# Kernel tuning notes

Hardware: AMD Instinct MI355X
Metric: run time of the kernel (lower is better)

The kernel has to match this reference:

```python
import jax, jax.numpy as jnp
import numpy as np

N = 50000       # nodes
E = 800000      # directed edges (src -> dst)
INDIM, HID, OUT = 256, 128, 64
NEG_SLOPE = 0.2  # PyG GATConv default negative_slope


def gat_layer(x, src, dst, W, a_src, a_dst, b, n_nodes):
    """Single-head PyG-style GATConv with self-loops already in (src, dst)."""
    h = x @ W.T                                   # [N, F_out]
    alpha_src = h @ a_src                         # [N]
    alpha_dst = h @ a_dst                         # [N]
    # per-edge attention logits, LeakyReLU
    e = jax.nn.leaky_relu(alpha_src[src] + alpha_dst[dst], NEG_SLOPE)  # [E']
    # segment softmax grouped by destination node (numerically stable)
    m = jnp.full((n_nodes,), -jnp.inf, e.dtype).at[dst].max(e)
    ee = jnp.exp(e - m[dst])
    denom = jax.ops.segment_sum(ee, dst, num_segments=n_nodes)
    alpha = ee / denom[dst]                       # [E']
    # weighted scatter-add of source messages
    out = jax.ops.segment_sum(h[src] * alpha[:, None], dst, num_segments=n_nodes)
    return out + b


def setup_inputs() -> dict:
    key = jax.random.key(0)
    ks = jax.random.split(key, 10)
    s = 0.1
    return {
        "x": jax.random.normal(ks[0], (N, INDIM), jnp.float32),
        "edge_index": jax.random.randint(ks[1], (2, E), 0, N, dtype=jnp.int32),
        "W1": jax.random.normal(ks[2], (HID, INDIM), jnp.float32) * s,
        "a_src1": jax.random.normal(ks[3], (HID,), jnp.float32) * s,
        "a_dst1": jax.random.normal(ks[4], (HID,), jnp.float32) * s,
        "b1": jnp.zeros((HID,), jnp.float32),
        "W2": jax.random.normal(ks[5], (OUT, HID), jnp.float32) * s,
        "a_src2": jax.random.normal(ks[6], (OUT,), jnp.float32) * s,
        "a_dst2": jax.random.normal(ks[7], (OUT,), jnp.float32) * s,
        "b2": jnp.zeros((OUT,), jnp.float32),
    }


def reference(x, edge_index, W1, a_src1, a_dst1, b1, W2, a_src2, a_dst2, b2):
    n_nodes = x.shape[0]
    # PyG GATConv default add_self_loops=True
    loops = jnp.arange(n_nodes, dtype=edge_index.dtype)
    src = jnp.concatenate([edge_index[0], loops])
    dst = jnp.concatenate([edge_index[1], loops])
    h = gat_layer(x, src, dst, W1, a_src1, a_dst1, b1, n_nodes)
    h = jax.nn.relu(h)
    h = gat_layer(h, src, dst, W2, a_src2, a_dst2, b2, n_nodes)
    return h
```

## Files before the change

kernel.cpp:

```cpp
#include <hip/hip_runtime.h>
#include <hip/hip_bf16.h>
#include <math.h>

#define NN 50000
#define EE 800000
#define INDIM 256
#define HID 128
#define OUTF 64
#define NEG_SLOPE 0.2f
#define CAP 64
#define SCHUNK 2048

typedef __attribute__((ext_vector_type(8))) short bf16x8;
typedef __attribute__((ext_vector_type(4))) float f32x4;

__device__ inline float bflo(unsigned p) { return __uint_as_float(p << 16); }
__device__ inline float bfhi(unsigned p) { return __uint_as_float(p & 0xffff0000u); }
__device__ inline unsigned f2bf(float f) {
    unsigned u = __float_as_uint(f);
    return (u + 0x7fffu + ((u >> 16) & 1u)) >> 16;
}
__device__ inline float leaky(float l) { return (l > 0.f) ? l : NEG_SLOPE * l; }

template <typename AT, int BN, int WR, int WC, bool FA>
__device__ inline void gemm_body(const AT* __restrict__ A,
                                 const float* __restrict__ B,
                                 unsigned short* __restrict__ Cb,
                                 const float* __restrict__ a_s,
                                 const float* __restrict__ a_d,
                                 float* __restrict__ asrc,
                                 float* __restrict__ adst,
                                 int N, int K, int bid)
{
    constexpr int BM = 128, LD = 40;
    constexpr int MF = (BM / WR) / 16;
    constexpr int NF = (BN / WC) / 16;
    static_assert(!FA || WC == 1, "register alpha needs full cols per wave");
    __shared__ unsigned short As[BM * LD];
    __shared__ unsigned short Bs[BN * LD];

    const int tid = threadIdx.x;
    const int wave = tid >> 6, lane = tid & 63;
    const int wr = wave / WC, wc = wave % WC;
    const int wrow0 = wr * (BM / WR);
    const int wcol0 = wc * (BN / WC);
    const int row0 = bid * BM;
    const int lrow = lane & 15, lkg = lane >> 4;

    f32x4 acc[MF][NF];
    #pragma unroll
    for (int mi = 0; mi < MF; ++mi)
        #pragma unroll
        for (int ni = 0; ni < NF; ++ni) acc[mi][ni] = 0.f;

    for (int k0 = 0; k0 < K; k0 += 32) {
        if constexpr (sizeof(AT) == 4) {
            #pragma unroll
            for (int i = tid; i < BM * 8; i += 256) {
                int row = i >> 3, kq = i & 7;
                float4 v = make_float4(0.f, 0.f, 0.f, 0.f);
                int gr = row0 + row;
                if (gr < N) v = *(const float4*)((const float*)A + (size_t)gr * K + k0 + kq * 4);
                unsigned p0 = f2bf(v.x) | (f2bf(v.y) << 16);
                unsigned p1 = f2bf(v.z) | (f2bf(v.w) << 16);
                *(uint2*)&As[row * LD + kq * 4] = make_uint2(p0, p1);
            }
        } else {
            #pragma unroll
            for (int i = tid; i < BM * 4; i += 256) {
                int row = i >> 2, q = i & 3;
                uint4 v = make_uint4(0u, 0u, 0u, 0u);
                int gr = row0 + row;
                if (gr < N) v = *(const uint4*)((const unsigned short*)A + (size_t)gr * K + k0 + q * 8);
                *(uint4*)&As[row * LD + q * 8] = v;
            }
        }
        #pragma unroll
        for (int i = tid; i < BN * 8; i += 256) {
            int row = i >> 3, kq = i & 7;
            float4 v = *(const float4*)(B + (size_t)row * K + k0 + kq * 4);
            unsigned p0 = f2bf(v.x) | (f2bf(v.y) << 16);
            unsigned p1 = f2bf(v.z) | (f2bf(v.w) << 16);
            *(uint2*)&Bs[row * LD + kq * 4] = make_uint2(p0, p1);
        }
        __syncthreads();

        bf16x8 af[MF], bfr[NF];
        #pragma unroll
        for (int mi = 0; mi < MF; ++mi)
            af[mi] = *(const bf16x8*)&As[(wrow0 + mi * 16 + lrow) * LD + lkg * 8];
        #pragma unroll
        for (int ni = 0; ni < NF; ++ni)
            bfr[ni] = *(const bf16x8*)&Bs[(wcol0 + ni * 16 + lrow) * LD + lkg * 8];
        #pragma unroll
        for (int mi = 0; mi < MF; ++mi)
            #pragma unroll
            for (int ni = 0; ni < NF; ++ni)
                acc[mi][ni] = __builtin_amdgcn_mfma_f32_16x16x32_bf16(
                    af[mi], bfr[ni], acc[mi][ni], 0, 0, 0);
        __syncthreads();
    }

    if constexpr (FA) {
        float asv[NF], adv[NF];
        #pragma unroll
        for (int ni = 0; ni < NF; ++ni) {
            int c = ni * 16 + lrow;
            asv[ni] = a_s[c]; adv[ni] = a_d[c];
        }
        #pragma unroll
        for (int mi = 0; mi < MF; ++mi)
            #pragma unroll
            for (int r = 0; r < 4; ++r) {
                float ps = 0.f, pd = 0.f;
                #pragma unroll
                for (int ni = 0; ni < NF; ++ni) {
                    ps = fmaf(acc[mi][ni][r], asv[ni], ps);
                    pd = fmaf(acc[mi][ni][r], adv[ni], pd);
                }
                #pragma unroll
                for (int d = 1; d < 16; d <<= 1) {
                    ps += __shfl_xor(ps, d);
                    pd += __shfl_xor(pd, d);
                }
                int gr = row0 + wrow0 + mi * 16 + lkg * 4 + r;
                if (lrow == 0 && gr < N) { asrc[gr] = ps; adst[gr] = pd; }
            }
    }

    #pragma unroll
    for (int mi = 0; mi < MF; ++mi)
        #pragma unroll
        for (int ni = 0; ni < NF; ++ni)
            #pragma unroll
            for (int r = 0; r < 4; ++r) {
                int gr = row0 + wrow0 + mi * 16 + lkg * 4 + r;
                int gc = wcol0 + ni * 16 + lrow;
                if (gr < N)
                    Cb[(size_t)gr * BN + gc] = (unsigned short)f2bf(acc[mi][ni][r]);
            }
}

__global__ __launch_bounds__(256) void fused_gemm1_scatter(
    const float* __restrict__ x, const float* __restrict__ W1,
    unsigned short* __restrict__ h1b,
    const int* __restrict__ src_in, const int* __restrict__ dst_in,
    int* __restrict__ cnt, unsigned short* __restrict__ csr,
    int N, int K, int GB, int E)
{
    if ((int)blockIdx.x < GB) {
        gemm_body<float, 128, 2, 2, false>(x, W1, h1b, nullptr, nullptr,
                                           nullptr, nullptr, N, K, blockIdx.x);
    } else {
        const int sb = (int)blockIdx.x - GB;
        const int cls = sb & 7;
        const int base_e = (sb >> 3) * SCHUNK;
        const int tot = E + N;
        #pragma unroll
        for (int j = 0; j < SCHUNK / 256; ++j) {
            int e = base_e + j * 256 + (int)threadIdx.x;
            if (e < tot) {
                int d = (e < E) ? dst_in[e] : (e - E);
                if (((d >> 12) & 7) == cls) {
                    int s = (e < E) ? src_in[e] : d;
                    int r = atomicAdd(&cnt[d], 1);
                    if (r < CAP) csr[((size_t)d << 6) + r] = (unsigned short)s;
                }
            }
        }
    }
}

__global__ __launch_bounds__(256) void gemm2_alpha_kernel(
    const unsigned short* __restrict__ A, const float* __restrict__ B,
    unsigned short* __restrict__ Cb,
    const float* __restrict__ a_s, const float* __restrict__ a_d,
    float* __restrict__ asrc, float* __restrict__ adst, int N, int K)
{
    gemm_body<unsigned short, 64, 4, 1, true>(A, B, Cb, a_s, a_d,
                                              asrc, adst, N, K, blockIdx.x);
}

template <int F>
__global__ __launch_bounds__(256) void alpha_kernel(
    const unsigned short* __restrict__ hb, const float* __restrict__ a_src,
    const float* __restrict__ a_dst, float* __restrict__ asrc,
    float* __restrict__ adst, int n)
{
    int wave = (int)((blockIdx.x * (size_t)blockDim.x + threadIdx.x) >> 6);
    int lane = threadIdx.x & 63;
    if (wave >= n) return;
    float p1 = 0.f, p2 = 0.f;
    if (F == 128 || lane < 32) {
        unsigned q = *(const unsigned*)(hb + (size_t)wave * F + lane * 2);
        float f0 = bflo(q), f1 = bfhi(q);
        p1 = f0 * a_src[lane * 2] + f1 * a_src[lane * 2 + 1];
        p2 = f0 * a_dst[lane * 2] + f1 * a_dst[lane * 2 + 1];
    }
    #pragma unroll
    for (int d = 32; d > 0; d >>= 1) {
        p1 += __shfl_xor(p1, d);
        p2 += __shfl_xor(p2, d);
    }
    if (lane == 0) { asrc[wave] = p1; adst[wave] = p2; }
}

template <int F, bool RELU, bool OUTBF>
__global__ __launch_bounds__(256) void aggregate_kernel(
    const unsigned short* __restrict__ hb, const unsigned short* __restrict__ csr,
    const int* __restrict__ cnt_arr, const float* __restrict__ asrc,
    const float* __restrict__ adst, const float* __restrict__ bias,
    void* __restrict__ outv, int n)
{
    constexpr int G = F / 8;
    constexpr int EPI = 64 / G;
    int wave = (int)((blockIdx.x * (size_t)blockDim.x + threadIdx.x) >> 6);
    int lane = threadIdx.x & 63;
    if (wave >= n) return;
    const size_t beg = (size_t)wave << 6;
    int cntv = cnt_arr[wave];
    cntv = (cntv > CAP) ? CAP : cntv;
    const float ad = adst[wave];
    const int grp = lane / G, fl = lane % G;

    float acc[8];
    #pragma unroll
    for (int p = 0; p < 8; ++p) acc[p] = 0.f;

    {
        int s = 0;
        float e = 0.f;
        if (lane < cntv) { s = (int)csr[beg + lane]; e = __expf(leaky(asrc[s] + ad)); }
        float denom = e;
        #pragma unroll
        for (int d = 32; d > 0; d >>= 1) denom += __shfl_xor(denom, d);
        float w = e * __fdividef(1.f, denom);
        for (int jj = 0; jj < cntv; jj += EPI) {
            int sel = jj + grp;
            int sj = __shfl(s, sel);
            float wj = __shfl(w, sel);
            uint4 q = *(const uint4*)(hb + (size_t)sj * F + fl * 8);
            acc[0] += wj * bflo(q.x); acc[1] += wj * bfhi(q.x);
            acc[2] += wj * bflo(q.y); acc[3] += wj * bfhi(q.y);
            acc[4] += wj * bflo(q.z); acc[5] += wj * bfhi(q.z);
            acc[6] += wj * bflo(q.w); acc[7] += wj * bfhi(q.w);
        }
    }

    #pragma unroll
    for (int d = G; d < 64; d <<= 1)
        #pragma unroll
        for (int p = 0; p < 8; ++p) acc[p] += __shfl_xor(acc[p], d);

    if (lane < G) {
        float v[8];
        #pragma unroll
        for (int p = 0; p < 8; ++p) {
            v[p] = acc[p] + bias[fl * 8 + p];
            if (RELU) v[p] = fmaxf(v[p], 0.f);
        }
        if constexpr (OUTBF) {
            unsigned short* o = (unsigned short*)outv + (size_t)wave * F + fl * 8;
            uint4 pk;
            pk.x = f2bf(v[0]) | (f2bf(v[1]) << 16);
            pk.y = f2bf(v[2]) | (f2bf(v[3]) << 16);
            pk.z = f2bf(v[4]) | (f2bf(v[5]) << 16);
            pk.w = f2bf(v[6]) | (f2bf(v[7]) << 16);
            *(uint4*)o = pk;
        } else {
            float* o = (float*)outv + (size_t)wave * F + fl * 8;
            *(float4*)o       = make_float4(v[0], v[1], v[2], v[3]);
            *(float4*)(o + 4) = make_float4(v[4], v[5], v[6], v[7]);
        }
    }
}

extern "C" void kernel_launch(void* const* d_in, const int* in_sizes, int n_in,
                              void* d_out, int out_size, void* d_ws, size_t ws_size,
                              hipStream_t stream)
{
    const float* x      = (const float*)d_in[0];
    const int*   ei     = (const int*)d_in[1];
    const float* W1     = (const float*)d_in[2];
    const float* a_src1 = (const float*)d_in[3];
    const float* a_dst1 = (const float*)d_in[4];
    const float* b1     = (const float*)d_in[5];
    const float* W2     = (const float*)d_in[6];
    const float* a_src2 = (const float*)d_in[7];
    const float* a_dst2 = (const float*)d_in[8];
    const float* b2     = (const float*)d_in[9];
    float* out = (float*)d_out;

    const int N = NN, E = EE;
    const int* src_in = ei;
    const int* dst_in = ei + E;

    char* p = (char*)d_ws;
    unsigned short* h1b   = (unsigned short*)p; p += (size_t)N * HID * 2;
    unsigned short* hmidb = (unsigned short*)p; p += (size_t)N * HID * 2;
    unsigned short* h2b   = (unsigned short*)p; p += (size_t)N * OUTF * 2;
    float* asrc = (float*)p; p += (size_t)N * 4;
    float* adst = (float*)p; p += (size_t)N * 4;
    int* cnt    = (int*)p;   p += (size_t)N * 4;
    unsigned short* csr = (unsigned short*)p; p += (size_t)N * CAP * 2;

    hipMemsetAsync(cnt, 0, (size_t)N * 4, stream);

    const int GB = (N + 127) / 128;
    const int SB = 8 * ((E + N + SCHUNK - 1) / SCHUNK);
    const int nwb = (N * 64 + 255) / 256;

    fused_gemm1_scatter<<<GB + SB, 256, 0, stream>>>(
        x, W1, h1b, src_in, dst_in, cnt, csr, N, INDIM, GB, E);
    alpha_kernel<HID><<<nwb, 256, 0, stream>>>(h1b, a_src1, a_dst1, asrc, adst, N);
    aggregate_kernel<HID, true, true><<<nwb, 256, 0, stream>>>(
        h1b, csr, cnt, asrc, adst, b1, hmidb, N);

    gemm2_alpha_kernel<<<GB, 256, 0, stream>>>(hmidb, W2, h2b, a_src2, a_dst2,
                                               asrc, adst, N, HID);
    aggregate_kernel<OUTF, false, false><<<nwb, 256, 0, stream>>>(
        h2b, csr, cnt, asrc, adst, b2, out, N);

    (void)in_sizes; (void)n_in; (void)out_size; (void)ws_size;
}
```

Measured before the change: 241.7 us.

## Fuse layer-1 alpha into GEMM, simplify CSR scatter, batch aggregate loads

```diff
diff --git a/kernel.cpp b/kernel.cpp
--- a/kernel.cpp
+++ b/kernel.cpp
@@ -9,7 +9,6 @@
 #define OUTF 64
 #define NEG_SLOPE 0.2f
 #define CAP 64
-#define SCHUNK 2048
 
 typedef __attribute__((ext_vector_type(8))) short bf16x8;
 typedef __attribute__((ext_vector_type(4))) float f32x4;
@@ -22,7 +21,7 @@
 }
 __device__ inline float leaky(float l) { return (l > 0.f) ? l : NEG_SLOPE * l; }
 
-template <typename AT, int BN, int WR, int WC, bool FA>
+template <typename AT, int BN, int WR, int WC, bool FA, bool FAL>
 __device__ inline void gemm_body(const AT* __restrict__ A,
                                  const float* __restrict__ B,
                                  unsigned short* __restrict__ Cb,
@@ -38,6 +37,7 @@
     static_assert(!FA || WC == 1, "register alpha needs full cols per wave");
     __shared__ unsigned short As[BM * LD];
     __shared__ unsigned short Bs[BN * LD];
+    __shared__ float al_s[FAL ? 2 * BM : 2];
 
     const int tid = threadIdx.x;
     const int wave = tid >> 6, lane = tid & 63;
@@ -46,6 +46,10 @@
     const int wcol0 = wc * (BN / WC);
     const int row0 = bid * BM;
     const int lrow = lane & 15, lkg = lane >> 4;
+
+    if constexpr (FAL) {
+        for (int i = tid; i < 2 * BM; i += 256) al_s[i] = 0.f;
+    }
 
     f32x4 acc[MF][NF];
     #pragma unroll
@@ -101,11 +105,11 @@
         __syncthreads();
     }
 
-    if constexpr (FA) {
+    if constexpr (FA || FAL) {
         float asv[NF], adv[NF];
         #pragma unroll
         for (int ni = 0; ni < NF; ++ni) {
-            int c = ni * 16 + lrow;
+            int c = wcol0 + ni * 16 + lrow;
             asv[ni] = a_s[c]; adv[ni] = a_d[c];
         }
         #pragma unroll
@@ -123,8 +127,16 @@
                     ps += __shfl_xor(ps, d);
                     pd += __shfl_xor(pd, d);
                 }
-                int gr = row0 + wrow0 + mi * 16 + lkg * 4 + r;
-                if (lrow == 0 && gr < N) { asrc[gr] = ps; adst[gr] = pd; }
+                int lr_ = wrow0 + mi * 16 + lkg * 4 + r;
+                if constexpr (FA) {
+                    int gr = row0 + lr_;
+                    if (lrow == 0 && gr < N) { asrc[gr] = ps; adst[gr] = pd; }
+                } else {
+                    if (lrow == 0) {
+                        atomicAdd(&al_s[lr_], ps);
+                        atomicAdd(&al_s[BM + lr_], pd);
+                    }
+                }
             }
     }
 
@@ -139,35 +151,37 @@
                 if (gr < N)
                     Cb[(size_t)gr * BN + gc] = (unsigned short)f2bf(acc[mi][ni][r]);
             }
+
+    if constexpr (FAL) {
+        __syncthreads();
+        if (tid < BM) {
+            int gr = row0 + tid;
+            if (gr < N) { asrc[gr] = al_s[tid]; adst[gr] = al_s[BM + tid]; }
+        }
+    }
 }
 
 __global__ __launch_bounds__(256) void fused_gemm1_scatter(
     const float* __restrict__ x, const float* __restrict__ W1,
     unsigned short* __restrict__ h1b,
+    const float* __restrict__ a_s, const float* __restrict__ a_d,
+    float* __restrict__ asrc, float* __restrict__ adst,
     const int* __restrict__ src_in, const int* __restrict__ dst_in,
     int* __restrict__ cnt, unsigned short* __restrict__ csr,
     int N, int K, int GB, int E)
 {
     if ((int)blockIdx.x < GB) {
-        gemm_body<float, 128, 2, 2, false>(x, W1, h1b, nullptr, nullptr,
-                                           nullptr, nullptr, N, K, blockIdx.x);
+        gemm_body<float, 128, 2, 2, false, true>(x, W1, h1b, a_s, a_d,
+                                                 asrc, adst, N, K, blockIdx.x);
     } else {
-        const int sb = (int)blockIdx.x - GB;
-        const int cls = sb & 7;
-        const int base_e = (sb >> 3) * SCHUNK;
-        const int tot = E + N;
-        #pragma unroll
-        for (int j = 0; j < SCHUNK / 256; ++j) {
-            int e = base_e + j * 256 + (int)threadIdx.x;
-            if (e < tot) {
-                int d = (e < E) ? dst_in[e] : (e - E);
-                if (((d >> 12) & 7) == cls) {
-                    int s = (e < E) ? src_in[e] : d;
-                    int r = atomicAdd(&cnt[d], 1);
-                    if (r < CAP) csr[((size_t)d << 6) + r] = (unsigned short)s;
-                }
-            }
-        }
+        int e = (blockIdx.x - GB) * 256 + threadIdx.x;
+        int tot = E + N;
+        if (e >= tot) return;
+        int d, s;
+        if (e < E) { d = dst_in[e]; s = src_in[e]; }
+        else       { d = e - E;    s = d; }
+        int r = atomicAdd(&cnt[d], 1);
+        if (r < CAP) csr[((size_t)d << 6) + r] = (unsigned short)s;
     }
 }
 
@@ -177,32 +191,8 @@
     const float* __restrict__ a_s, const float* __restrict__ a_d,
     float* __restrict__ asrc, float* __restrict__ adst, int N, int K)
 {
-    gemm_body<unsigned short, 64, 4, 1, true>(A, B, Cb, a_s, a_d,
-                                              asrc, adst, N, K, blockIdx.x);
-}
-
-template <int F>
-__global__ __launch_bounds__(256) void alpha_kernel(
-    const unsigned short* __restrict__ hb, const float* __restrict__ a_src,
-    const float* __restrict__ a_dst, float* __restrict__ asrc,
-    float* __restrict__ adst, int n)
-{
-    int wave = (int)((blockIdx.x * (size_t)blockDim.x + threadIdx.x) >> 6);
-    int lane = threadIdx.x & 63;
-    if (wave >= n) return;
-    float p1 = 0.f, p2 = 0.f;
-    if (F == 128 || lane < 32) {
-        unsigned q = *(const unsigned*)(hb + (size_t)wave * F + lane * 2);
-        float f0 = bflo(q), f1 = bfhi(q);
-        p1 = f0 * a_src[lane * 2] + f1 * a_src[lane * 2 + 1];
-        p2 = f0 * a_dst[lane * 2] + f1 * a_dst[lane * 2 + 1];
-    }
-    #pragma unroll
-    for (int d = 32; d > 0; d >>= 1) {
-        p1 += __shfl_xor(p1, d);
-        p2 += __shfl_xor(p2, d);
-    }
-    if (lane == 0) { asrc[wave] = p1; adst[wave] = p2; }
+    gemm_body<unsigned short, 64, 4, 1, true, false>(A, B, Cb, a_s, a_d,
+                                                     asrc, adst, N, K, blockIdx.x);
 }
 
 template <int F, bool RELU, bool OUTBF>
@@ -214,6 +204,7 @@
 {
     constexpr int G = F / 8;
     constexpr int EPI = 64 / G;
+    constexpr int STEP = EPI * 4;
     int wave = (int)((blockIdx.x * (size_t)blockDim.x + threadIdx.x) >> 6);
     int lane = threadIdx.x & 63;
     if (wave >= n) return;
@@ -227,23 +218,32 @@
     #pragma unroll
     for (int p = 0; p < 8; ++p) acc[p] = 0.f;
 
-    {
-        int s = 0;
-        float e = 0.f;
-        if (lane < cntv) { s = (int)csr[beg + lane]; e = __expf(leaky(asrc[s] + ad)); }
-        float denom = e;
-        #pragma unroll
-        for (int d = 32; d > 0; d >>= 1) denom += __shfl_xor(denom, d);
-        float w = e * __fdividef(1.f, denom);
-        for (int jj = 0; jj < cntv; jj += EPI) {
-            int sel = jj + grp;
+    int s = 0;
+    float e = 0.f;
+    if (lane < cntv) { s = (int)csr[beg + lane]; e = __expf(leaky(asrc[s] + ad)); }
+    float denom = e;
+    #pragma unroll
+    for (int d = 32; d > 0; d >>= 1) denom += __shfl_xor(denom, d);
+    float w = e * __fdividef(1.f, denom);
+
+    for (int jj0 = 0; jj0 < cntv; jj0 += STEP) {
+        uint4 q[4];
+        float wj[4];
+        #pragma unroll
+        for (int u = 0; u < 4; ++u) {
+            int sel = jj0 + u * EPI + grp;
             int sj = __shfl(s, sel);
-            float wj = __shfl(w, sel);
-            uint4 q = *(const uint4*)(hb + (size_t)sj * F + fl * 8);
-            acc[0] += wj * bflo(q.x); acc[1] += wj * bfhi(q.x);
-            acc[2] += wj * bflo(q.y); acc[3] += wj * bfhi(q.y);
-            acc[4] += wj * bflo(q.z); acc[5] += wj * bfhi(q.z);
-            acc[6] += wj * bflo(q.w); acc[7] += wj * bfhi(q.w);
+            wj[u] = __shfl(w, sel);
+            q[u] = make_uint4(0u, 0u, 0u, 0u);
+            if (sel < cntv)
+                q[u] = *(const uint4*)(hb + (size_t)sj * F + fl * 8);
+        }
+        #pragma unroll
+        for (int u = 0; u < 4; ++u) {
+            acc[0] += wj[u] * bflo(q[u].x); acc[1] += wj[u] * bfhi(q[u].x);
+            acc[2] += wj[u] * bflo(q[u].y); acc[3] += wj[u] * bfhi(q[u].y);
+            acc[4] += wj[u] * bflo(q[u].z); acc[5] += wj[u] * bfhi(q[u].z);
+            acc[6] += wj[u] * bflo(q[u].w); acc[7] += wj[u] * bfhi(q[u].w);
         }
     }
 
@@ -307,12 +307,12 @@
     hipMemsetAsync(cnt, 0, (size_t)N * 4, stream);
 
     const int GB = (N + 127) / 128;
-    const int SB = 8 * ((E + N + SCHUNK - 1) / SCHUNK);
+    const int SB = (E + N + 255) / 256;
     const int nwb = (N * 64 + 255) / 256;
 
     fused_gemm1_scatter<<<GB + SB, 256, 0, stream>>>(
-        x, W1, h1b, src_in, dst_in, cnt, csr, N, INDIM, GB, E);
-    alpha_kernel<HID><<<nwb, 256, 0, stream>>>(h1b, a_src1, a_dst1, asrc, adst, N);
+        x, W1, h1b, a_src1, a_dst1, asrc, adst, src_in, dst_in, cnt, csr,
+        N, INDIM, GB, E);
     aggregate_kernel<HID, true, true><<<nwb, 256, 0, stream>>>(
         h1b, csr, cnt, asrc, adst, b1, hmidb, N);
 
```

Result: faster. 232.6 us (-3.7%).
